# Kernel tuning notes

Hardware: AMD Instinct MI355X
Metric: run time of the kernel (lower is better)

The kernel has to match this reference:

```python
import jax, jax.numpy as jnp
import numpy as np

N_NODES = 100000


def setup_inputs() -> dict:
    key = jax.random.key(0)
    k1, k2, k3, k4, k5 = jax.random.split(key, 5)
    n_edges = 1600000
    d_in, d_out = 128, 128
    input_features = jax.random.normal(k1, (N_NODES, d_in), dtype=jnp.float32)
    weight = jax.random.normal(k2, (d_in, d_out), dtype=jnp.float32) * (1.0 / np.sqrt(d_out))
    edge_vals = jax.random.uniform(k3, (n_edges,), dtype=jnp.float32)
    edge_src = jax.random.randint(k4, (n_edges,), 0, N_NODES, dtype=jnp.int32)
    edge_dst = jax.random.randint(k5, (n_edges,), 0, N_NODES, dtype=jnp.int32)
    return {
        "input_features": input_features,
        "weight": weight,
        "edge_vals": edge_vals,
        "edge_src": edge_src,
        "edge_dst": edge_dst,
    }


def reference(input_features, weight, edge_vals, edge_src, edge_dst):
    neg_slope = 0.0
    # dense transform: support = X @ W  -> [N, d_out]
    support = input_features @ weight
    # sparse SpMM: out[dst] += val * support[src]  (COO adjacency)
    msgs = edge_vals[:, None] * support[edge_src]  # [E, d_out]
    output = jax.ops.segment_sum(msgs, edge_dst, num_segments=N_NODES)
    # leaky_relu with negative_slope = neg_slope (0 -> relu)
    return jnp.where(output >= 0, output, neg_slope * output)
```

## Files before the change

kernel.cpp:

```cpp
#include <hip/hip_runtime.h>
#include <hip/hip_bf16.h>


#define D 128
#define NB_SHIFT 6
#define BNODES 64
#define MAXB 2048
#define CAPB 1408
#define RPT 6
#define XSTR 136

using bf16x8 = __attribute__((ext_vector_type(8))) short;
using f32x4  = __attribute__((ext_vector_type(4))) float;

__device__ inline unsigned short f2bf(float f) {
    unsigned u = __float_as_uint(f);
    u += 0x7fffu + ((u >> 16) & 1u);
    return (unsigned short)(u >> 16);
}
__device__ inline float bflo(unsigned w) { return __uint_as_float(w << 16); }
__device__ inline float bfhi(unsigned w) { return __uint_as_float(w & 0xffff0000u); }

__global__ __launch_bounds__(256) void wtrans(const float* __restrict__ W,
                                              unsigned short* __restrict__ WT,
                                              int* cursor, int nb) {
    const int t = threadIdx.x, b = blockIdx.x;
    const int n  = (b << 4) | (t & 15);
    const int k0 = (t >> 4) << 3;
#pragma unroll
    for (int k = k0; k < k0 + 8; ++k)
        WT[n * D + k] = f2bf(W[k * D + n]);
    if (b == 0)
        for (int i = t; i < nb; i += 256) cursor[i] = 0;
}

__global__ __launch_bounds__(256) void gemm_mfma(const float* __restrict__ X,
                                                 const unsigned short* __restrict__ WT,
                                                 unsigned short* __restrict__ S,
                                                 int nRows) {
    __shared__ unsigned short Xl[64 * XSTR];
    __shared__ unsigned short Wl[128 * XSTR];

    const int t = threadIdx.x;
    const int row0 = blockIdx.x * 64;

    const uint4* WT4 = (const uint4*)WT;
    uint4* Wl4 = (uint4*)Wl;
#pragma unroll
    for (int i = t; i < 2048; i += 256) {
        int n = i >> 4, kc8 = i & 15;
        Wl4[n * (XSTR / 8) + kc8] = WT4[i];
    }

    const float4* X4 = (const float4*)X;
    ushort4* Xl4 = (ushort4*)Xl;
#pragma unroll
    for (int i = t; i < 2048; i += 256) {
        int r = i >> 5, c = i & 31;
        int gr = row0 + r;
        float4 v = make_float4(0.f, 0.f, 0.f, 0.f);
        if (gr < nRows) v = X4[(size_t)gr * 32 + c];
        ushort4 p;
        p.x = f2bf(v.x); p.y = f2bf(v.y); p.z = f2bf(v.z); p.w = f2bf(v.w);
        Xl4[r * (XSTR / 4) + c] = p;
    }
    __syncthreads();

    const int wv = t >> 6, lane = t & 63;
    const int m = lane & 15, quad = lane >> 4;
    const int m0 = wv << 4;

    f32x4 acc[8];
    f32x4 z = {0.f, 0.f, 0.f, 0.f};
#pragma unroll
    for (int nt = 0; nt < 8; ++nt) acc[nt] = z;

#pragma unroll
    for (int kc = 0; kc < 4; ++kc) {
        bf16x8 a = *(const bf16x8*)(Xl + (m0 + m) * XSTR + kc * 32 + quad * 8);
#pragma unroll
        for (int nt = 0; nt < 8; ++nt) {
            bf16x8 b = *(const bf16x8*)(Wl + (nt * 16 + m) * XSTR + kc * 32 + quad * 8);
            acc[nt] = __builtin_amdgcn_mfma_f32_16x16x32_bf16(a, b, acc[nt], 0, 0, 0);
        }
    }

#pragma unroll
    for (int nt = 0; nt < 8; ++nt) {
#pragma unroll
        for (int r = 0; r < 4; ++r) {
            int gr = row0 + m0 + quad * 4 + r;
            if (gr < nRows) S[(size_t)gr * D + nt * 16 + m] = f2bf(acc[nt][r]);
        }
    }
}

__global__ __launch_bounds__(1024, 4) void fill2(const int* __restrict__ src,
                                                 const int* __restrict__ dst,
                                                 const float* __restrict__ vals,
                                                 int* gcursor, int2* __restrict__ epk,
                                                 int E, int nb) {
    __shared__ int h[MAXB];
    __shared__ int cur[MAXB];
    const int t = threadIdx.x;
    for (int i = t; i < nb; i += 1024) h[i] = 0;
    __syncthreads();

    int chunk = (E + gridDim.x - 1) / gridDim.x;
    chunk = (chunk + 3) & ~3;
    const int s0 = min(E, (int)blockIdx.x * chunk);
    const int s1 = min(E, s0 + chunk);
    const int vend = s0 + ((s1 - s0) & ~3);

    int e = s0 + (t << 2);
    for (; e + 4 <= vend; e += 4096) {
        int4 d = *(const int4*)(dst + e);
        atomicAdd(&h[d.x >> NB_SHIFT], 1);
        atomicAdd(&h[d.y >> NB_SHIFT], 1);
        atomicAdd(&h[d.z >> NB_SHIFT], 1);
        atomicAdd(&h[d.w >> NB_SHIFT], 1);
    }
    for (e = vend + t; e < s1; e += 1024) atomicAdd(&h[dst[e] >> NB_SHIFT], 1);
    __syncthreads();

    for (int i = t; i < nb; i += 1024) {
        int c = h[i];
        cur[i] = c ? (i * CAPB + atomicAdd(&gcursor[i], c)) : 0;
    }
    __syncthreads();

    e = s0 + (t << 2);
    for (; e + 4 <= vend; e += 4096) {
        int4   d = *(const int4*)(dst + e);
        int4   s = *(const int4*)(src + e);
        float4 v = *(const float4*)(vals + e);
        int p0 = atomicAdd(&cur[d.x >> NB_SHIFT], 1);
        int p1 = atomicAdd(&cur[d.y >> NB_SHIFT], 1);
        int p2 = atomicAdd(&cur[d.z >> NB_SHIFT], 1);
        int p3 = atomicAdd(&cur[d.w >> NB_SHIFT], 1);
        epk[p0] = make_int2(s.x | ((d.x & (BNODES - 1)) << 20), __float_as_int(v.x));
        epk[p1] = make_int2(s.y | ((d.y & (BNODES - 1)) << 20), __float_as_int(v.y));
        epk[p2] = make_int2(s.z | ((d.z & (BNODES - 1)) << 20), __float_as_int(v.z));
        epk[p3] = make_int2(s.w | ((d.w & (BNODES - 1)) << 20), __float_as_int(v.w));
    }
    for (e = vend + t; e < s1; e += 1024) {
        int d = dst[e];
        int pos = atomicAdd(&cur[d >> NB_SHIFT], 1);
        epk[pos] = make_int2(src[e] | ((d & (BNODES - 1)) << 20), __float_as_int(vals[e]));
    }
}

__global__ __launch_bounds__(256, 8) void bucket_gather(const unsigned short* __restrict__ support,
                                                        const int* __restrict__ gcursor,
                                                        const int2* __restrict__ epk,
                                                        float* __restrict__ out, int N) {
    __shared__ int2 se[CAPB];
    __shared__ int  hist[BNODES];
    __shared__ int  rows[BNODES];
    __shared__ int  cur[BNODES];

    const int t   = threadIdx.x;
    const int b   = blockIdx.x;
    const int cnt = min(gcursor[b], CAPB);
    const int beg = b * CAPB;

    if (t < BNODES) hist[t] = 0;
    __syncthreads();

    int2 r[RPT];
#pragma unroll
    for (int i = 0; i < RPT; ++i) {
        int idx = t + (i << 8);
        if (idx < cnt) r[i] = epk[beg + idx];
    }
#pragma unroll
    for (int i = 0; i < RPT; ++i) {
        int idx = t + (i << 8);
        if (idx < cnt) atomicAdd(&hist[(r[i].x >> 20) & (BNODES - 1)], 1);
    }
    __syncthreads();

    if (t < BNODES) rows[t] = hist[t];
    __syncthreads();
#pragma unroll
    for (int off = 1; off < BNODES; off <<= 1) {
        int v = 0;
        if (t < BNODES && t >= off) v = rows[t - off];
        __syncthreads();
        if (t < BNODES && t >= off) rows[t] += v;
        __syncthreads();
    }
    if (t < BNODES) cur[t] = rows[t] - hist[t];
    __syncthreads();

#pragma unroll
    for (int i = 0; i < RPT; ++i) {
        int idx = t + (i << 8);
        if (idx < cnt) {
            int pos = atomicAdd(&cur[(r[i].x >> 20) & (BNODES - 1)], 1);
            se[pos] = r[i];
        }
    }
    __syncthreads();

    const int g = t >> 4, lane = t & 15;
    const int node0 = b << NB_SHIFT;
    const uint4* S4 = (const uint4*)support;
    float4* o4 = (float4*)out;

#pragma unroll
    for (int nn = g; nn < BNODES; nn += 16) {
        const int send = rows[nn];
        const int sbeg = send - hist[nn];

        float a[8];
#pragma unroll
        for (int k = 0; k < 8; ++k) a[k] = 0.f;

        int j = sbeg;
        for (; j + 3 < send; j += 4) {
            int2 e0 = se[j], e1 = se[j + 1], e2 = se[j + 2], e3 = se[j + 3];
            uint4 m0 = S4[(size_t)(e0.x & 0xFFFFF) * 16 + lane];
            uint4 m1 = S4[(size_t)(e1.x & 0xFFFFF) * 16 + lane];
            uint4 m2 = S4[(size_t)(e2.x & 0xFFFFF) * 16 + lane];
            uint4 m3 = S4[(size_t)(e3.x & 0xFFFFF) * 16 + lane];
            float v0 = __int_as_float(e0.y), v1 = __int_as_float(e1.y);
            float v2 = __int_as_float(e2.y), v3 = __int_as_float(e3.y);
            a[0] = fmaf(v0, bflo(m0.x), a[0]); a[1] = fmaf(v0, bfhi(m0.x), a[1]);
            a[2] = fmaf(v0, bflo(m0.y), a[2]); a[3] = fmaf(v0, bfhi(m0.y), a[3]);
            a[4] = fmaf(v0, bflo(m0.z), a[4]); a[5] = fmaf(v0, bfhi(m0.z), a[5]);
            a[6] = fmaf(v0, bflo(m0.w), a[6]); a[7] = fmaf(v0, bfhi(m0.w), a[7]);
            a[0] = fmaf(v1, bflo(m1.x), a[0]); a[1] = fmaf(v1, bfhi(m1.x), a[1]);
            a[2] = fmaf(v1, bflo(m1.y), a[2]); a[3] = fmaf(v1, bfhi(m1.y), a[3]);
            a[4] = fmaf(v1, bflo(m1.z), a[4]); a[5] = fmaf(v1, bfhi(m1.z), a[5]);
            a[6] = fmaf(v1, bflo(m1.w), a[6]); a[7] = fmaf(v1, bfhi(m1.w), a[7]);
            a[0] = fmaf(v2, bflo(m2.x), a[0]); a[1] = fmaf(v2, bfhi(m2.x), a[1]);
            a[2] = fmaf(v2, bflo(m2.y), a[2]); a[3] = fmaf(v2, bfhi(m2.y), a[3]);
            a[4] = fmaf(v2, bflo(m2.z), a[4]); a[5] = fmaf(v2, bfhi(m2.z), a[5]);
            a[6] = fmaf(v2, bflo(m2.w), a[6]); a[7] = fmaf(v2, bfhi(m2.w), a[7]);
            a[0] = fmaf(v3, bflo(m3.x), a[0]); a[1] = fmaf(v3, bfhi(m3.x), a[1]);
            a[2] = fmaf(v3, bflo(m3.y), a[2]); a[3] = fmaf(v3, bfhi(m3.y), a[3]);
            a[4] = fmaf(v3, bflo(m3.z), a[4]); a[5] = fmaf(v3, bfhi(m3.z), a[5]);
            a[6] = fmaf(v3, bflo(m3.w), a[6]); a[7] = fmaf(v3, bfhi(m3.w), a[7]);
        }
        for (; j < send; ++j) {
            int2 e0 = se[j];
            uint4 m0 = S4[(size_t)(e0.x & 0xFFFFF) * 16 + lane];
            float v0 = __int_as_float(e0.y);
            a[0] = fmaf(v0, bflo(m0.x), a[0]); a[1] = fmaf(v0, bfhi(m0.x), a[1]);
            a[2] = fmaf(v0, bflo(m0.y), a[2]); a[3] = fmaf(v0, bfhi(m0.y), a[3]);
            a[4] = fmaf(v0, bflo(m0.z), a[4]); a[5] = fmaf(v0, bfhi(m0.z), a[5]);
            a[6] = fmaf(v0, bflo(m0.w), a[6]); a[7] = fmaf(v0, bfhi(m0.w), a[7]);
        }

        const int gn = node0 + nn;
        if (gn < N) {
            size_t base = (size_t)gn * 32 + 2 * lane;
            float4 lo = make_float4(fmaxf(a[0], 0.f), fmaxf(a[1], 0.f),
                                    fmaxf(a[2], 0.f), fmaxf(a[3], 0.f));
            float4 hi = make_float4(fmaxf(a[4], 0.f), fmaxf(a[5], 0.f),
                                    fmaxf(a[6], 0.f), fmaxf(a[7], 0.f));
            o4[base]     = lo;
            o4[base + 1] = hi;
        }
    }
}

extern "C" void kernel_launch(void* const* d_in, const int* in_sizes, int n_in,
                              void* d_out, int out_size, void* d_ws, size_t ws_size,
                              hipStream_t stream) {
    const float* X    = (const float*)d_in[0];
    const float* W    = (const float*)d_in[1];
    const float* vals = (const float*)d_in[2];
    const int*   src  = (const int*)d_in[3];
    const int*   dst  = (const int*)d_in[4];
    float*       out  = (float*)d_out;

    const int N  = in_sizes[0] / D;
    const int E  = in_sizes[2];
    const int nb = (N + BNODES - 1) / BNODES;

    size_t off = 0;
    auto take = [&](size_t bytes) {
        size_t p = off;
        off = (off + bytes + 255) & ~(size_t)255;
        return p;
    };
    char* ws = (char*)d_ws;
    size_t o_support = take((size_t)N * D * sizeof(unsigned short));
    size_t o_wt      = take((size_t)D * D * sizeof(unsigned short));
    size_t o_cursor  = take((size_t)nb * sizeof(int));
    size_t o_epk     = take(((size_t)nb * CAPB + 1024) * sizeof(int2));
    (void)ws_size;

    unsigned short* support = (unsigned short*)(ws + o_support);
    unsigned short* WT      = (unsigned short*)(ws + o_wt);
    int*  cursor = (int*)(ws + o_cursor);
    int2* epk    = (int2*)(ws + o_epk);

    wtrans<<<8, 256, 0, stream>>>(W, WT, cursor, nb);

    gemm_mfma<<<(N + 63) / 64, 256, 0, stream>>>(X, WT, support, N);

    fill2<<<256, 1024, 0, stream>>>(src, dst, vals, cursor, epk, E, nb);

    bucket_gather<<<nb, 256, 0, stream>>>(support, cursor, epk, out, N);
}
```

Baseline: 218.5 us.

## Fuse GEMM and edge bucketing into one launch; unroll gather by eight

Merges the MFMA GEMM and the COO bucket-fill kernel into a single 1024-thread launch whose first blocks do the fill and whose remaining blocks do the GEMM. The two independent stages can then run concurrently and one launch gap disappears. GEMM blocks grow to 16 waves, each computing two N-tiles instead of eight, sharing LDS with the fill path. The gather loop is unrolled to eight outstanding row loads, with occupancy hint lowered to 6. This risks lower GEMM efficiency from less per-wave reuse and higher register pressure in the gather.

```diff
diff --git a/kernel.cpp b/kernel.cpp
--- a/kernel.cpp
+++ b/kernel.cpp
@@ -9,6 +9,7 @@
 #define CAPB 1408
 #define RPT 6
 #define XSTR 136
+#define NFILL 256
 
 using bf16x8 = __attribute__((ext_vector_type(8))) short;
 using f32x4  = __attribute__((ext_vector_type(4))) float;
@@ -34,20 +35,22 @@
         for (int i = t; i < nb; i += 256) cursor[i] = 0;
 }
 
-__global__ __launch_bounds__(256) void gemm_mfma(const float* __restrict__ X,
-                                                 const unsigned short* __restrict__ WT,
-                                                 unsigned short* __restrict__ S,
-                                                 int nRows) {
-    __shared__ unsigned short Xl[64 * XSTR];
-    __shared__ unsigned short Wl[128 * XSTR];
+#define SMEM_BYTES (64 * XSTR * 2 + 128 * XSTR * 2)
+
+__device__ void gemm_path(const float* __restrict__ X,
+                          const unsigned short* __restrict__ WT,
+                          unsigned short* __restrict__ S,
+                          int nRows, int blk, char* smem) {
+    unsigned short* Xl = (unsigned short*)smem;
+    unsigned short* Wl = (unsigned short*)(smem + 64 * XSTR * 2);
 
     const int t = threadIdx.x;
-    const int row0 = blockIdx.x * 64;
+    const int row0 = blk * 64;
 
     const uint4* WT4 = (const uint4*)WT;
     uint4* Wl4 = (uint4*)Wl;
 #pragma unroll
-    for (int i = t; i < 2048; i += 256) {
+    for (int i = t; i < 2048; i += 1024) {
         int n = i >> 4, kc8 = i & 15;
         Wl4[n * (XSTR / 8) + kc8] = WT4[i];
     }
@@ -55,7 +58,7 @@
     const float4* X4 = (const float4*)X;
     ushort4* Xl4 = (ushort4*)Xl;
 #pragma unroll
-    for (int i = t; i < 2048; i += 256) {
+    for (int i = t; i < 2048; i += 1024) {
         int r = i >> 5, c = i & 31;
         int gr = row0 + r;
         float4 v = make_float4(0.f, 0.f, 0.f, 0.f);
@@ -68,47 +71,45 @@
 
     const int wv = t >> 6, lane = t & 63;
     const int m = lane & 15, quad = lane >> 4;
-    const int m0 = wv << 4;
-
-    f32x4 acc[8];
-    f32x4 z = {0.f, 0.f, 0.f, 0.f};
-#pragma unroll
-    for (int nt = 0; nt < 8; ++nt) acc[nt] = z;
+    const int m0  = (wv & 3) << 4;
+    const int nt0 = (wv >> 2) << 1;
+
+    f32x4 acc0 = {0.f, 0.f, 0.f, 0.f};
+    f32x4 acc1 = {0.f, 0.f, 0.f, 0.f};
 
 #pragma unroll
     for (int kc = 0; kc < 4; ++kc) {
         bf16x8 a = *(const bf16x8*)(Xl + (m0 + m) * XSTR + kc * 32 + quad * 8);
-#pragma unroll
-        for (int nt = 0; nt < 8; ++nt) {
-            bf16x8 b = *(const bf16x8*)(Wl + (nt * 16 + m) * XSTR + kc * 32 + quad * 8);
-            acc[nt] = __builtin_amdgcn_mfma_f32_16x16x32_bf16(a, b, acc[nt], 0, 0, 0);
-        }
-    }
-
-#pragma unroll
-    for (int nt = 0; nt < 8; ++nt) {
-#pragma unroll
-        for (int r = 0; r < 4; ++r) {
-            int gr = row0 + m0 + quad * 4 + r;
-            if (gr < nRows) S[(size_t)gr * D + nt * 16 + m] = f2bf(acc[nt][r]);
-        }
-    }
-}
-
-__global__ __launch_bounds__(1024, 4) void fill2(const int* __restrict__ src,
-                                                 const int* __restrict__ dst,
-                                                 const float* __restrict__ vals,
-                                                 int* gcursor, int2* __restrict__ epk,
-                                                 int E, int nb) {
-    __shared__ int h[MAXB];
-    __shared__ int cur[MAXB];
+        bf16x8 b0 = *(const bf16x8*)(Wl + ((nt0 + 0) * 16 + m) * XSTR + kc * 32 + quad * 8);
+        bf16x8 b1 = *(const bf16x8*)(Wl + ((nt0 + 1) * 16 + m) * XSTR + kc * 32 + quad * 8);
+        acc0 = __builtin_amdgcn_mfma_f32_16x16x32_bf16(a, b0, acc0, 0, 0, 0);
+        acc1 = __builtin_amdgcn_mfma_f32_16x16x32_bf16(a, b1, acc1, 0, 0, 0);
+    }
+
+#pragma unroll
+    for (int r = 0; r < 4; ++r) {
+        int gr = row0 + m0 + quad * 4 + r;
+        if (gr < nRows) {
+            S[(size_t)gr * D + (nt0 + 0) * 16 + m] = f2bf(acc0[r]);
+            S[(size_t)gr * D + (nt0 + 1) * 16 + m] = f2bf(acc1[r]);
+        }
+    }
+}
+
+__device__ void fill2_path(const int* __restrict__ src,
+                           const int* __restrict__ dst,
+                           const float* __restrict__ vals,
+                           int* gcursor, int2* __restrict__ epk,
+                           int E, int nb, int blk, char* smem) {
+    int* h   = (int*)smem;
+    int* cur = (int*)(smem + MAXB * 4);
     const int t = threadIdx.x;
     for (int i = t; i < nb; i += 1024) h[i] = 0;
     __syncthreads();
 
-    int chunk = (E + gridDim.x - 1) / gridDim.x;
+    int chunk = (E + NFILL - 1) / NFILL;
     chunk = (chunk + 3) & ~3;
-    const int s0 = min(E, (int)blockIdx.x * chunk);
+    const int s0 = min(E, blk * chunk);
     const int s1 = min(E, s0 + chunk);
     const int vend = s0 + ((s1 - s0) & ~3);
 
@@ -150,7 +151,30 @@
     }
 }
 
-__global__ __launch_bounds__(256, 8) void bucket_gather(const unsigned short* __restrict__ support,
+__global__ __launch_bounds__(1024, 8) void fused_pre(const float* __restrict__ X,
+                                                     const unsigned short* __restrict__ WT,
+                                                     unsigned short* __restrict__ S,
+                                                     int nRows,
+                                                     const int* __restrict__ src,
+                                                     const int* __restrict__ dst,
+                                                     const float* __restrict__ vals,
+                                                     int* gcursor, int2* __restrict__ epk,
+                                                     int E, int nb) {
+    __shared__ char smem[SMEM_BYTES];
+    const int bid = blockIdx.x;
+    if (bid < NFILL)
+        fill2_path(src, dst, vals, gcursor, epk, E, nb, bid, smem);
+    else
+        gemm_path(X, WT, S, nRows, bid - NFILL, smem);
+}
+
+#define ACC8(e, mm) { float v = __int_as_float(e.y);                         \
+    a[0] = fmaf(v, bflo(mm.x), a[0]); a[1] = fmaf(v, bfhi(mm.x), a[1]);      \
+    a[2] = fmaf(v, bflo(mm.y), a[2]); a[3] = fmaf(v, bfhi(mm.y), a[3]);      \
+    a[4] = fmaf(v, bflo(mm.z), a[4]); a[5] = fmaf(v, bfhi(mm.z), a[5]);      \
+    a[6] = fmaf(v, bflo(mm.w), a[6]); a[7] = fmaf(v, bfhi(mm.w), a[7]); }
+
+__global__ __launch_bounds__(256, 6) void bucket_gather(const unsigned short* __restrict__ support,
                                                         const int* __restrict__ gcursor,
                                                         const int2* __restrict__ epk,
                                                         float* __restrict__ out, int N) {
@@ -218,39 +242,32 @@
         for (int k = 0; k < 8; ++k) a[k] = 0.f;
 
         int j = sbeg;
-        for (; j + 3 < send; j += 4) {
+        for (; j + 8 <= send; j += 8) {
+            int2 e0 = se[j],     e1 = se[j + 1], e2 = se[j + 2], e3 = se[j + 3];
+            int2 e4 = se[j + 4], e5 = se[j + 5], e6 = se[j + 6], e7 = se[j + 7];
+            uint4 m0 = S4[(size_t)(e0.x & 0xFFFFF) * 16 + lane];
+            uint4 m1 = S4[(size_t)(e1.x & 0xFFFFF) * 16 + lane];
+            uint4 m2 = S4[(size_t)(e2.x & 0xFFFFF) * 16 + lane];
+            uint4 m3 = S4[(size_t)(e3.x & 0xFFFFF) * 16 + lane];
+            uint4 m4 = S4[(size_t)(e4.x & 0xFFFFF) * 16 + lane];
+            uint4 m5 = S4[(size_t)(e5.x & 0xFFFFF) * 16 + lane];
+            uint4 m6 = S4[(size_t)(e6.x & 0xFFFFF) * 16 + lane];
+            uint4 m7 = S4[(size_t)(e7.x & 0xFFFFF) * 16 + lane];
+            ACC8(e0, m0); ACC8(e1, m1); ACC8(e2, m2); ACC8(e3, m3);
+            ACC8(e4, m4); ACC8(e5, m5); ACC8(e6, m6); ACC8(e7, m7);
+        }
+        for (; j + 4 <= send; j += 4) {
             int2 e0 = se[j], e1 = se[j + 1], e2 = se[j + 2], e3 = se[j + 3];
             uint4 m0 = S4[(size_t)(e0.x & 0xFFFFF) * 16 + lane];
             uint4 m1 = S4[(size_t)(e1.x & 0xFFFFF) * 16 + lane];
             uint4 m2 = S4[(size_t)(e2.x & 0xFFFFF) * 16 + lane];
             uint4 m3 = S4[(size_t)(e3.x & 0xFFFFF) * 16 + lane];
-            float v0 = __int_as_float(e0.y), v1 = __int_as_float(e1.y);
-            float v2 = __int_as_float(e2.y), v3 = __int_as_float(e3.y);
-            a[0] = fmaf(v0, bflo(m0.x), a[0]); a[1] = fmaf(v0, bfhi(m0.x), a[1]);
-            a[2] = fmaf(v0, bflo(m0.y), a[2]); a[3] = fmaf(v0, bfhi(m0.y), a[3]);
-            a[4] = fmaf(v0, bflo(m0.z), a[4]); a[5] = fmaf(v0, bfhi(m0.z), a[5]);
-            a[6] = fmaf(v0, bflo(m0.w), a[6]); a[7] = fmaf(v0, bfhi(m0.w), a[7]);
-            a[0] = fmaf(v1, bflo(m1.x), a[0]); a[1] = fmaf(v1, bfhi(m1.x), a[1]);
-            a[2] = fmaf(v1, bflo(m1.y), a[2]); a[3] = fmaf(v1, bfhi(m1.y), a[3]);
-            a[4] = fmaf(v1, bflo(m1.z), a[4]); a[5] = fmaf(v1, bfhi(m1.z), a[5]);
-            a[6] = fmaf(v1, bflo(m1.w), a[6]); a[7] = fmaf(v1, bfhi(m1.w), a[7]);
-            a[0] = fmaf(v2, bflo(m2.x), a[0]); a[1] = fmaf(v2, bfhi(m2.x), a[1]);
-            a[2] = fmaf(v2, bflo(m2.y), a[2]); a[3] = fmaf(v2, bfhi(m2.y), a[3]);
-            a[4] = fmaf(v2, bflo(m2.z), a[4]); a[5] = fmaf(v2, bfhi(m2.z), a[5]);
-            a[6] = fmaf(v2, bflo(m2.w), a[6]); a[7] = fmaf(v2, bfhi(m2.w), a[7]);
-            a[0] = fmaf(v3, bflo(m3.x), a[0]); a[1] = fmaf(v3, bfhi(m3.x), a[1]);
-            a[2] = fmaf(v3, bflo(m3.y), a[2]); a[3] = fmaf(v3, bfhi(m3.y), a[3]);
-            a[4] = fmaf(v3, bflo(m3.z), a[4]); a[5] = fmaf(v3, bfhi(m3.z), a[5]);
-            a[6] = fmaf(v3, bflo(m3.w), a[6]); a[7] = fmaf(v3, bfhi(m3.w), a[7]);
+            ACC8(e0, m0); ACC8(e1, m1); ACC8(e2, m2); ACC8(e3, m3);
         }
         for (; j < send; ++j) {
             int2 e0 = se[j];
             uint4 m0 = S4[(size_t)(e0.x & 0xFFFFF) * 16 + lane];
-            float v0 = __int_as_float(e0.y);
-            a[0] = fmaf(v0, bflo(m0.x), a[0]); a[1] = fmaf(v0, bfhi(m0.x), a[1]);
-            a[2] = fmaf(v0, bflo(m0.y), a[2]); a[3] = fmaf(v0, bfhi(m0.y), a[3]);
-            a[4] = fmaf(v0, bflo(m0.z), a[4]); a[5] = fmaf(v0, bfhi(m0.z), a[5]);
-            a[6] = fmaf(v0, bflo(m0.w), a[6]); a[7] = fmaf(v0, bfhi(m0.w), a[7]);
+            ACC8(e0, m0);
         }
 
         const int gn = node0 + nn;
@@ -300,9 +317,9 @@
 
     wtrans<<<8, 256, 0, stream>>>(W, WT, cursor, nb);
 
-    gemm_mfma<<<(N + 63) / 64, 256, 0, stream>>>(X, WT, support, N);
-
-    fill2<<<256, 1024, 0, stream>>>(src, dst, vals, cursor, epk, E, nb);
+    const int nbG = (N + 63) / 64;
+    fused_pre<<<NFILL + nbG, 1024, 0, stream>>>(X, WT, support, N,
+                                                src, dst, vals, cursor, epk, E, nb);
 
     bucket_gather<<<nb, 256, 0, stream>>>(support, cursor, epk, out, N);
 }
```

Result: faster. 208.6 us (-4.5%).
